# Performance work log

Hardware: AMD Instinct MI355X
Metric: run time of the kernel (lower is better)

The kernel has to match this reference:

```python
import jax, jax.numpy as jnp
import numpy as np

DIM = 2048
HQ = 32
HKV = 8
HEAD_DIM = DIM // HQ          # 64
GROUP = HQ // HKV             # 4 q-heads per kv-head
B, S = 2, 2048


def setup_inputs() -> dict:
    key = jax.random.key(0)
    ks = jax.random.split(key, 12)
    sc_in = 1.0 / np.sqrt(DIM)   # lecun_normal fan-in scaling
    inp = {
        "q": jax.random.normal(ks[0], (B, S, DIM), jnp.float32),
        "k": jax.random.normal(ks[1], (B, S, DIM), jnp.float32),
        "v": jax.random.normal(ks[2], (B, S, DIM), jnp.float32),
        # causal 0/1 mask: module computes scores -= 1/mask + 1, so 0 -> -inf (masked), 1 -> -2 (softmax-invariant shift)
        "mask": jnp.tril(jnp.ones((S, S), jnp.int32)),
        "Wq": jax.random.normal(ks[3], (DIM, HQ * HEAD_DIM), jnp.float32) * sc_in,
        "bq": jnp.zeros((HQ * HEAD_DIM,), jnp.float32),
        "Wk": jax.random.normal(ks[4], (DIM, HKV * HEAD_DIM), jnp.float32) * sc_in,
        "bk": jnp.zeros((HKV * HEAD_DIM,), jnp.float32),
        "Wv": jax.random.normal(ks[5], (DIM, HKV * HEAD_DIM), jnp.float32) * sc_in,
        "bv": jnp.zeros((HKV * HEAD_DIM,), jnp.float32),
        "Wo": jax.random.normal(ks[6], (DIM, DIM), jnp.float32) * (1.0 / np.sqrt(DIM)),
        "bo": jnp.zeros((DIM,), jnp.float32),
    }
    return inp


def reference(q, k, v, mask, Wq, bq, Wk, bk, Wv, bv, Wo, bo):
    b, s, _ = q.shape
    # projections -> per-head layout
    qx = (q @ Wq + bq).reshape(b, s, HKV, GROUP, HEAD_DIM)   # grouped q-heads
    kx = (k @ Wk + bk).reshape(b, s, HKV, HEAD_DIM)
    vx = (v @ Wv + bv).reshape(b, s, HKV, HEAD_DIM)
    # scores[b, h, g, i, j] = q_i . k_j ; same math as repeating kv heads GROUP times
    scores = jnp.einsum('bihgd,bjhd->bhgij', qx, kx) / jnp.sqrt(
        jnp.asarray(HEAD_DIM, qx.dtype))
    # module's masking: scores -= 1/mask + 1  (mask==0 -> -inf, mask==1 -> -2)
    scores = scores - (1.0 / mask.astype(scores.dtype) + 1.0)
    probs = jax.nn.softmax(scores, axis=-1)
    out = jnp.einsum('bhgij,bjhd->bihgd', probs, vx).reshape(b, s, DIM)
    out = out @ Wo + bo
    return out
```

## Files before the change

kernel.cpp:

```cpp
#include <hip/hip_runtime.h>

typedef unsigned short u16;
typedef unsigned int u32;
typedef __attribute__((ext_vector_type(8))) short short8v;
typedef __attribute__((ext_vector_type(4))) float f32x4;

#define DIM 2048
#define HQN 32
#define HKVN 8
#define HD 64
#define BB 2
#define SS 2048
#define MTOT (BB*SS)
#define NKV (HKVN*HD)
#define QSCL 0.18033688011112042f

__device__ __forceinline__ u16 f2bf(float f){
  u32 u = __float_as_uint(f);
  u += 0x7FFFu + ((u >> 16) & 1u);
  return (u16)(u >> 16);
}

__device__ __forceinline__ u32 cvtpk(float a, float b){
  u32 r; asm("v_cvt_pk_bf16_f32 %0, %1, %2" : "=v"(r) : "v"(a), "v"(b)); return r;
}

__device__ __forceinline__ void gload_lds16(const void* g, void* l){
  __builtin_amdgcn_global_load_lds((const __attribute__((address_space(1))) u32*)g,
                                   (__attribute__((address_space(3))) u32*)l, 16, 0, 0);
}

#define WAITVM_(N) asm volatile("s_waitcnt vmcnt(" #N ")" ::: "memory")
#define WAITVM(N) WAITVM_(N)
#define BARF()    do { asm volatile("" ::: "memory"); __builtin_amdgcn_s_barrier(); asm volatile("" ::: "memory"); } while(0)
#define MF(a,b,cc) __builtin_amdgcn_mfma_f32_16x16x32_bf16((a),(b),(cc),0,0,0)

__global__ __launch_bounds__(256) void cast3_kernel(const float4* __restrict__ q,
                                                    const float4* __restrict__ k,
                                                    const float4* __restrict__ v,
                                                    u16* __restrict__ qo,
                                                    u16* __restrict__ ko,
                                                    u16* __restrict__ vo, int n4){
  const int z = blockIdx.y;
  const float4* in = z==0 ? q : (z==1 ? k : v);
  u16* out = z==0 ? qo : (z==1 ? ko : vo);
  int i = blockIdx.x*256 + threadIdx.x;
  if (i < n4){
    float4 f = in[i];
    union { u16 s[4]; unsigned long long u; } r;
    r.s[0]=f2bf(f.x); r.s[1]=f2bf(f.y); r.s[2]=f2bf(f.z); r.s[3]=f2bf(f.w);
    *(unsigned long long*)(out + (size_t)i*4) = r.u;
  }
}

__global__ __launch_bounds__(256) void transpose4_kernel(const float* __restrict__ Wq,
                                                         const float* __restrict__ Wk,
                                                         const float* __restrict__ Wv,
                                                         const float* __restrict__ Wo,
                                                         u16* __restrict__ WqT,
                                                         u16* __restrict__ WkT,
                                                         u16* __restrict__ WvT,
                                                         u16* __restrict__ WoT){
  const int z = blockIdx.z;
  const float* W = z==0?Wq:(z==1?Wk:(z==2?Wv:Wo));
  u16* WT = z==0?WqT:(z==1?WkT:(z==2?WvT:WoT));
  const int N = (z==1||z==2) ? NKV : DIM;
  const int K = DIM;
  int n0 = blockIdx.x*32, k0 = blockIdx.y*32;
  if (n0 >= N) return;
  __shared__ float tile[32][33];
  int tx = threadIdx.x & 31, ty = threadIdx.x >> 5;
  #pragma unroll
  for (int i=0;i<4;i++){
    int kk = ty + i*8;
    tile[kk][tx] = W[(size_t)(k0+kk)*N + n0 + tx];
  }
  __syncthreads();
  #pragma unroll
  for (int i=0;i<4;i++){
    int n = ty + i*8;
    WT[(size_t)(n0+n)*K + k0 + tx] = f2bf(tile[tx][n]);
  }
}

__global__ __launch_bounds__(512, 1) void gemm_qkv_kernel(const u16* __restrict__ Aq,
                                                          const u16* __restrict__ Ak,
                                                          const u16* __restrict__ Av,
                                                          const u16* __restrict__ BT,
                                                          const float* __restrict__ bq,
                                                          const float* __restrict__ bk,
                                                          const float* __restrict__ bv,
                                                          u16* __restrict__ Qp,
                                                          u16* __restrict__ Kp,
                                                          u16* __restrict__ Vp){
  __shared__ __align__(16) u16 lds[65536];
  char* ldsb = (char*)lds;
  const int t = threadIdx.x, lane = t & 63, w = t >> 6;
  const int wm = w >> 2, wn = w & 3, g = lane >> 4, c = lane & 15;
  int bid = blockIdx.x;
  bid = (bid & 7)*24 + (bid >> 3);
  const int mt = bid / 12, nt = bid - mt*12;
  const int m0 = mt*256, n0 = nt*256;
  const int seg = (n0 >= 2560) ? 2 : (n0 >= 2048 ? 1 : 0);
  const u16* A = seg==0 ? Aq : (seg==1 ? Ak : Av);
  const float* bias = seg==0 ? bq : (seg==1 ? bk : bv);
  const int nbase = seg==0 ? 0 : (seg==1 ? 2048 : 2560);

  const int rA = t >> 3;
  const int kc = ((t & 7) ^ (rA & 7)) * 8;
  const u16* gA = A  + (size_t)(m0 + rA)*DIM + kc;
  const u16* gB = BT + (size_t)(n0 + ((rA>>5)<<6) + (rA & 31))*DIM + kc;

  const u32 ko0 = (u32)((g*16) ^ ((c&7)<<4));
  const u32 ko1 = (u32)((64 + g*16) ^ ((c&7)<<4));
  const u32 aoff = wm*8192 + c*128;
  const u32 boff = wn*4096 + c*128;

#define STGA_(PA, KT, ABASE) do{ \
    gload_lds16(gA + (size_t)(KT)*64 + (size_t)((PA)*64)*DIM,       ldsb + (ABASE) + (PA)*16384 + t*16); \
    gload_lds16(gA + (size_t)(KT)*64 + (size_t)((PA)*64+128)*DIM,   ldsb + (ABASE) + (PA)*16384 + 8192 + t*16); }while(0)
#define STGB_(PB, KT, BBASE) do{ \
    gload_lds16(gB + (size_t)(KT)*64 + (size_t)((PB)*32)*DIM,       ldsb + (BBASE) + (PB)*16384 + t*16); \
    gload_lds16(gB + (size_t)(KT)*64 + (size_t)((PB)*32+128)*DIM,   ldsb + (BBASE) + (PB)*16384 + 8192 + t*16); }while(0)
#define LD8(OFF) (*(const short8v*)(ldsb + (OFF)))

  const f32x4 fzero = {0.f,0.f,0.f,0.f};
  f32x4 acc[8][4];
  #pragma unroll
  for (int i=0;i<8;i++)
    #pragma unroll
    for (int j=0;j<4;j++) acc[i][j] = fzero;

#define RD_A(PABASE) do{ _Pragma("unroll") for (int q=0;q<4;q++){ \
    a_[q][0] = LD8((PABASE) + aoff + q*2048 + ko0); \
    a_[q][1] = LD8((PABASE) + aoff + q*2048 + ko1); } }while(0)
#define RD_B(DST, PBBASE) do{ _Pragma("unroll") for (int s=0;s<2;s++){ \
    DST[s][0] = LD8((PBBASE) + boff + s*2048 + ko0); \
    DST[s][1] = LD8((PBBASE) + boff + s*2048 + ko1); } }while(0)

#define MM16(BSRC, FM0, FN0) do{ __builtin_amdgcn_s_setprio(1); \
    _Pragma("unroll") for (int q=0;q<4;q++) \
      _Pragma("unroll") for (int s=0;s<2;s++){ \
        acc[(FM0)+q][(FN0)+s] = MF(a_[q][0], BSRC[s][0], acc[(FM0)+q][(FN0)+s]); \
        acc[(FM0)+q][(FN0)+s] = MF(a_[q][1], BSRC[s][1], acc[(FM0)+q][(FN0)+s]); } \
    __builtin_amdgcn_s_setprio(0); }while(0)

#define QSTEP(TT, CUR, DOSTG, TAIL) do{ \
    const u32 AC = (CUR)*32768,  BC2 = 65536 + (CUR)*32768; \
    const u32 AN = (CUR^1)*32768, BN2 = 65536 + (CUR^1)*32768; \
    short8v a_[4][2], b0_[2][2], b1_[2][2]; \
     \
    RD_A(AC); RD_B(b0_, BC2); \
    if (DOSTG) STGA_(0, (TT)+1, AN); \
    MM16(b0_, 0, 0); \
    if (TAIL) { WAITVM(2); } else { WAITVM(4); } \
    BARF(); \
     \
    RD_B(b1_, BC2 + 16384); \
    if (DOSTG) STGB_(0, (TT)+1, BN2); \
    MM16(b1_, 0, 2); \
    if (TAIL) { WAITVM(0); } else { WAITVM(4); } \
    BARF(); \
     \
    RD_A(AC + 16384); \
    if (DOSTG) STGB_(1, (TT)+1, BN2); \
    MM16(b1_, 4, 2); \
    BARF(); \
     \
    if (DOSTG) STGA_(1, (TT)+1, AN); \
    MM16(b0_, 4, 0); \
    if (!TAIL) { WAITVM(4); } \
    BARF(); \
  }while(0)

  STGA_(0, 0, 0); STGB_(0, 0, 65536); STGB_(1, 0, 65536); STGA_(1, 0, 0);
  WAITVM(4);
  BARF();

  #pragma unroll 1
  for (int tt = 0; tt < 30; tt += 2){
    QSTEP(tt,   0, 1, 0);
    QSTEP(tt+1, 1, 1, 0);
  }
  QSTEP(30, 0, 1, 0);
  QSTEP(31, 1, 0, 1);
#undef QSTEP

  WAITVM(0);
  __syncthreads();

  u16* st = lds + w*8192;
  const float osc = (seg == 0) ? QSCL : 1.0f;
  if (seg == 2){
    #pragma unroll
    for (int fm=0; fm<8; fm++){
      #pragma unroll
      for (int fn=0; fn<4; fn++){
        float bvv = bias[n0 - nbase + wn*64 + fn*16 + c];
        int vbase = (fm>>1)*2048 + fn*512 + (g*16 + c)*8 + (fm&1)*4;
        *(u32*)&st[vbase]     = cvtpk(acc[fm][fn][0]+bvv, acc[fm][fn][1]+bvv);
        *(u32*)&st[vbase + 2] = cvtpk(acc[fm][fn][2]+bvv, acc[fm][fn][3]+bvv);
      }
    }
  } else {
    #pragma unroll
    for (int fm=0; fm<8; fm++){
      #pragma unroll
      for (int fn=0; fn<4; fn++){
        float bvv = bias[n0 - nbase + wn*64 + fn*16 + c];
        int sbase = (fm>>1)*2048 + ((fm&1)*2 + (fn>>1))*512 + (c>>2)*128 + (fn&1)*4 + (c&3);
        #pragma unroll
        for (int r=0; r<4; r++)
          st[sbase + (4*g + r)*8] = f2bf((acc[fm][fn][r] + bvv)*osc);
      }
    }
  }
  __syncthreads();
  {
    const int bb = m0 >> 11;
    const int st0 = ((m0 & 2047) >> 5) + wm*4;
    u16* dst;
    if (seg == 0)      dst = Qp + (((size_t)bb*HQN  + (n0>>6)        + wn) << 17);
    else if (seg == 1) dst = Kp + (((size_t)bb*HKVN + ((n0-2048)>>6) + wn) << 17);
    else               dst = Vp + (((size_t)bb*HKVN + ((n0-2560)>>6) + wn) << 17);
    dst += (size_t)st0*2048;
    #pragma unroll
    for (int i=0;i<16;i++)
      *(short8v*)(dst + lane*8 + i*512) = *(const short8v*)(st + lane*8 + i*512);
  }
#undef STGA_
#undef STGB_
#undef RD_A
#undef RD_B
#undef MM16
#undef LD8
}

__global__ __launch_bounds__(512, 1) void gemm_o_kernel(const u16* __restrict__ A,
                                                        const u16* __restrict__ BT,
                                                        const float* __restrict__ bias,
                                                        float* __restrict__ C){
  __shared__ __align__(16) u16 lds[49152];
  char* ldsb = (char*)lds;
  const int t = threadIdx.x, lane = t & 63, w = t >> 6;
  const int wm = w >> 2, wn = w & 3, g = lane >> 4, c = lane & 15;
  int bid = blockIdx.x;
  bid = (bid & 7)*32 + (bid >> 3);
  const int m0 = (bid >> 4)*256, n0 = (bid & 15)*128;

  const int rA = t >> 3;
  const int kc = ((t & 7) ^ (rA & 7)) * 8;
  const u16* gA = A  + (size_t)(m0 + rA)*DIM + kc;
  const u16* gB = BT + (size_t)(n0 + rA)*DIM + kc;

  const u32 ko0 = (u32)((g*16) ^ ((c&7)<<4));
  const u32 ko1 = (u32)((64 + g*16) ^ ((c&7)<<4));
  const u32 aoff = wm*8192 + c*128;
  const u32 boffo = wn*4096 + c*128;

#define STGA_(PA, KT, ABASE) do{ \
    gload_lds16(gA + (size_t)(KT)*64 + (size_t)((PA)*64)*DIM,       ldsb + (ABASE) + (PA)*16384 + t*16); \
    gload_lds16(gA + (size_t)(KT)*64 + (size_t)((PA)*64+128)*DIM,   ldsb + (ABASE) + (PA)*16384 + 8192 + t*16); }while(0)
#define STGB_O(KT, BBASE) do{ \
    gload_lds16(gB + (size_t)(KT)*64,                     ldsb + (BBASE) + t*16); \
    gload_lds16(gB + (size_t)(KT)*64 + (size_t)64*DIM,    ldsb + (BBASE) + 8192 + t*16); }while(0)
#define LD8(OFF) (*(const short8v*)(ldsb + (OFF)))

  const f32x4 fzero = {0.f,0.f,0.f,0.f};
  f32x4 acc[8][2];
  #pragma unroll
  for (int i=0;i<8;i++){ acc[i][0] = fzero; acc[i][1] = fzero; }

#define RD_A(PABASE) do{ _Pragma("unroll") for (int q=0;q<4;q++){ \
    a_[q][0] = LD8((PABASE) + aoff + q*2048 + ko0); \
    a_[q][1] = LD8((PABASE) + aoff + q*2048 + ko1); } }while(0)
#define RD_BO(BBASE) do{ _Pragma("unroll") for (int s=0;s<2;s++){ \
    b_[s][0] = LD8((BBASE) + boffo + s*2048 + ko0); \
    b_[s][1] = LD8((BBASE) + boffo + s*2048 + ko1); } }while(0)

#define MMO(FM0) do{ __builtin_amdgcn_s_setprio(1); \
    _Pragma("unroll") for (int q=0;q<4;q++) \
      _Pragma("unroll") for (int s=0;s<2;s++){ \
        acc[(FM0)+q][s] = MF(a_[q][0], b_[s][0], acc[(FM0)+q][s]); \
        acc[(FM0)+q][s] = MF(a_[q][1], b_[s][1], acc[(FM0)+q][s]); } \
    __builtin_amdgcn_s_setprio(0); }while(0)

#define OSTEP(TT, CUR, DOSTG, TAIL) do{ \
    const u32 AC = (CUR)*32768,  BC2 = 65536 + (CUR)*16384; \
    const u32 AN = (CUR^1)*32768, BN2 = 65536 + (CUR^1)*16384; \
    short8v a_[4][2], b_[2][2]; \
     \
    RD_A(AC); RD_BO(BC2); \
    if (DOSTG) { STGA_(0, (TT)+1, AN); STGB_O((TT)+1, BN2); } \
    MMO(0); \
    if (TAIL) { WAITVM(0); } else { WAITVM(4); } \
    BARF(); \
     \
    RD_A(AC + 16384); \
    if (DOSTG) STGA_(1, (TT)+1, AN); \
    MMO(4); \
    if (!TAIL) { WAITVM(2); } \
    BARF(); \
  }while(0)

  STGA_(0, 0, 0); STGB_O(0, 65536); STGA_(1, 0, 0);
  WAITVM(2);
  BARF();

  #pragma unroll 1
  for (int tt = 0; tt < 30; tt += 2){
    OSTEP(tt,   0, 1, 0);
    OSTEP(tt+1, 1, 1, 0);
  }
  OSTEP(30, 0, 1, 0);
  OSTEP(31, 1, 0, 1);
#undef OSTEP

  #pragma unroll
  for (int fm=0; fm<8; fm++){
    #pragma unroll
    for (int s=0; s<2; s++){
      int n = n0 + wn*32 + s*16 + c;
      float bvv = bias[n];
      #pragma unroll
      for (int r=0; r<4; r++){
        int m = m0 + wm*128 + fm*16 + 4*g + r;
        C[(size_t)m*DIM + n] = acc[fm][s][r] + bvv;
      }
    }
  }
#undef STGA_
#undef STGB_O
#undef RD_A
#undef RD_BO
#undef MMO
#undef LD8
}

__global__ __launch_bounds__(256) void attn_kernel(const u16* __restrict__ Qp,
                                                   const u16* __restrict__ Kp,
                                                   const u16* __restrict__ Vp,
                                                   u16* __restrict__ Aout){
  const int bid = blockIdx.x;
  const int grp = bid & 15;
  const int T   = 63 - (bid >> 4);
  const int b   = grp >> 3;
  const int hkv = grp & 7;
  const int t = threadIdx.x;
  const int lane = t & 63, w = t >> 6;
  const int g = lane >> 4, c = lane & 15;
  const int hq = hkv*4 + w;

  __shared__ __align__(16) u16 ring[4][2][2048];

  const u16* Kb = Kp + (((size_t)b*HKVN + hkv) << 17);
  const u16* Vb = Vp + (((size_t)b*HKVN + hkv) << 17);
  const u16* Qb = Qp + (((size_t)b*HQN + hq) << 17);
  const f32x4 fzero = {0.f,0.f,0.f,0.f};

  short8v qf[2][2];
  {
    const u16* qs = Qb + (size_t)T*2048 + lane*8;
    qf[0][0] = *(const short8v*)(qs);
    qf[0][1] = *(const short8v*)(qs + 512);
    qf[1][0] = *(const short8v*)(qs + 1024);
    qf[1][1] = *(const short8v*)(qs + 1536);
  }
  float l_r[2] = {0.f, 0.f};
  f32x4 o[2][4];
  #pragma unroll
  for (int qi=0; qi<2; qi++)
    #pragma unroll
    for (int f=0; f<4; f++) o[qi][f] = fzero;

  #pragma unroll
  for (int s=0; s<3; s++){
    const int tc = s > T ? T : s;
    gload_lds16(Kb + (size_t)tc*2048 + t*8, &ring[s][0][t*8]);
    gload_lds16(Vb + (size_t)tc*2048 + t*8, &ring[s][1][t*8]);
  }

  for (int kt = 0; kt <= T; kt += 4){
    #pragma unroll
    for (int s4 = 0; s4 < 4; ++s4){
      const int kt_ = kt + s4;
      if (kt_ > T) break;
      WAITVM(4);
      BARF();
      short8v kf0 = *(const short8v*)&ring[s4][0][lane*8];
      short8v kf1 = *(const short8v*)&ring[s4][0][512 + lane*8];
      short8v kf2 = *(const short8v*)&ring[s4][0][1024 + lane*8];
      short8v kf3 = *(const short8v*)&ring[s4][0][1536 + lane*8];
      short8v vf0 = *(const short8v*)&ring[s4][1][lane*8];
      short8v vf1 = *(const short8v*)&ring[s4][1][512 + lane*8];
      short8v vf2 = *(const short8v*)&ring[s4][1][1024 + lane*8];
      short8v vf3 = *(const short8v*)&ring[s4][1][1536 + lane*8];
      {
        const int tc = (kt_+3) > T ? T : (kt_+3);
        const int sn = (s4+3) & 3;
        gload_lds16(Kb + (size_t)tc*2048 + t*8, &ring[sn][0][t*8]);
        gload_lds16(Vb + (size_t)tc*2048 + t*8, &ring[sn][1][t*8]);
      }
      const bool diag = (kt_ == T);
      #pragma unroll
      for (int qi=0; qi<2; qi++){
        f32x4 s0 = fzero, s1 = fzero;
        __builtin_amdgcn_s_setprio(1);
        s0 = MF(kf0, qf[qi][0], s0);
        s0 = MF(kf1, qf[qi][1], s0);
        s1 = MF(kf2, qf[qi][0], s1);
        s1 = MF(kf3, qf[qi][1], s1);
        __builtin_amdgcn_s_setprio(0);
        float p0[4], p1[4];
        #pragma unroll
        for (int r=0; r<4; r++){
          p0[r] = __builtin_amdgcn_exp2f(s0[r]);
          p1[r] = __builtin_amdgcn_exp2f(s1[r]);
        }
        if (diag){
          const int qloc = qi*16 + c;
          #pragma unroll
          for (int r=0; r<4; r++){
            if (4*g + r      > qloc) p0[r] = 0.f;
            if (16 + 4*g + r > qloc) p1[r] = 0.f;
          }
        }
        l_r[qi] += (p0[0]+p0[1]) + (p0[2]+p0[3]) + (p1[0]+p1[1]) + (p1[2]+p1[3]);
        union { u32 u[4]; short8v v; } pu;
        pu.u[0] = cvtpk(p0[0], p0[1]);
        pu.u[1] = cvtpk(p0[2], p0[3]);
        pu.u[2] = cvtpk(p1[0], p1[1]);
        pu.u[3] = cvtpk(p1[2], p1[3]);
        __builtin_amdgcn_s_setprio(1);
        o[qi][0] = MF(pu.v, vf0, o[qi][0]);
        o[qi][1] = MF(pu.v, vf1, o[qi][1]);
        o[qi][2] = MF(pu.v, vf2, o[qi][2]);
        o[qi][3] = MF(pu.v, vf3, o[qi][3]);
        __builtin_amdgcn_s_setprio(0);
      }
    }
  }

  #pragma unroll
  for (int qi=0; qi<2; qi++){
    float ls = l_r[qi];
    ls += __shfl_xor(ls, 16);
    ls += __shfl_xor(ls, 32);
    float li = 1.0f / ls;
    float lf[4];
    #pragma unroll
    for (int r=0; r<4; r++) lf[r] = __shfl(li, 4*g + r);
    #pragma unroll
    for (int f=0; f<4; f++){
      #pragma unroll
      for (int r=0; r<4; r++){
        int q = T*32 + qi*16 + 4*g + r;
        Aout[((size_t)b*SS + q)*DIM + hq*HD + f*16 + c] = f2bf(o[qi][f][r]*lf[r]);
      }
    }
  }
}

extern "C" void kernel_launch(void* const* d_in, const int* in_sizes, int n_in,
                              void* d_out, int out_size, void* d_ws, size_t ws_size,
                              hipStream_t stream){
  const float* q  = (const float*)d_in[0];
  const float* k  = (const float*)d_in[1];
  const float* v  = (const float*)d_in[2];
  const float* Wq = (const float*)d_in[4];
  const float* bq = (const float*)d_in[5];
  const float* Wk = (const float*)d_in[6];
  const float* bk = (const float*)d_in[7];
  const float* Wv = (const float*)d_in[8];
  const float* bv = (const float*)d_in[9];
  const float* Wo = (const float*)d_in[10];
  const float* bo = (const float*)d_in[11];
  float* out = (float*)d_out;

  char* ws = (char*)d_ws;
  u16* q_bf = (u16*)ws; ws += (size_t)MTOT*DIM*2;
  u16* k_bf = (u16*)ws; ws += (size_t)MTOT*DIM*2;
  u16* v_bf = (u16*)ws; ws += (size_t)MTOT*DIM*2;
  u16* WqT  = (u16*)ws; ws += (size_t)DIM*DIM*2;
  u16* WkT  = (u16*)ws; ws += (size_t)NKV*DIM*2;
  u16* WvT  = (u16*)ws; ws += (size_t)NKV*DIM*2;
  u16* WoT  = (u16*)ws; ws += (size_t)DIM*DIM*2;
  u16* Qp   = (u16*)ws; ws += (size_t)MTOT*DIM*2;
  u16* Kp   = (u16*)ws; ws += (size_t)MTOT*NKV*2;
  u16* Vp   = (u16*)ws; ws += (size_t)MTOT*NKV*2;
  u16* attn = (u16*)ws; ws += (size_t)MTOT*DIM*2;

  const int n4 = MTOT*DIM/4;
  cast3_kernel<<<dim3(n4/256, 3), 256, 0, stream>>>((const float4*)q, (const float4*)k,
                                                    (const float4*)v, q_bf, k_bf, v_bf, n4);
  transpose4_kernel<<<dim3(DIM/32, DIM/32, 4), 256, 0, stream>>>(Wq, Wk, Wv, Wo,
                                                                 WqT, WkT, WvT, WoT);
  gemm_qkv_kernel<<<192, 512, 0, stream>>>(q_bf, k_bf, v_bf, WqT,
                                           bq, bk, bv, Qp, Kp, Vp);
  attn_kernel<<<1024, 256, 0, stream>>>(Qp, Kp, Vp, attn);
  gemm_o_kernel<<<256, 512, 0, stream>>>(attn, WoT, bo, out);
}
```

Baseline: 188.4 us.

## Process two adjacent query tiles per attention block with 512 threads sharing K/V

Each attention block now has 8 waves covering two consecutive 32-row query tiles for the same kv-head, so every K/V tile staged in LDS serves twice as many waves. Global-to-LDS loading is split, with half the threads fetching K and half V. Block ordering is remapped so heavy and light tile pairs interleave. The grid is halved to 512 blocks, and waves of the lower tile sit idle for the final K/V step, which adds a little imbalance and lowers the number of independent blocks.

```diff
diff --git a/kernel.cpp b/kernel.cpp
--- a/kernel.cpp
+++ b/kernel.cpp
@@ -337,19 +337,23 @@
 #undef LD8
 }
 
-__global__ __launch_bounds__(256) void attn_kernel(const u16* __restrict__ Qp,
+__global__ __launch_bounds__(512) void attn_kernel(const u16* __restrict__ Qp,
                                                    const u16* __restrict__ Kp,
                                                    const u16* __restrict__ Vp,
                                                    u16* __restrict__ Aout){
   const int bid = blockIdx.x;
   const int grp = bid & 15;
-  const int T   = 63 - (bid >> 4);
+  const int j   = bid >> 4;
+  const int Tp  = (j < 16) ? j : 47 - j;
+  const int TB  = 2*Tp;
+  const int TMAX = TB + 1;
   const int b   = grp >> 3;
   const int hkv = grp & 7;
   const int t = threadIdx.x;
   const int lane = t & 63, w = t >> 6;
   const int g = lane >> 4, c = lane & 15;
-  const int hq = hkv*4 + w;
+  const int hq = hkv*4 + (w & 3);
+  const int Tw = TB + (w >> 2);
 
   __shared__ __align__(16) u16 ring[4][2][2048];
 
@@ -360,7 +364,7 @@
 
   short8v qf[2][2];
   {
-    const u16* qs = Qb + (size_t)T*2048 + lane*8;
+    const u16* qs = Qb + (size_t)Tw*2048 + lane*8;
     qf[0][0] = *(const short8v*)(qs);
     qf[0][1] = *(const short8v*)(qs + 512);
     qf[1][0] = *(const short8v*)(qs + 1024);
@@ -375,68 +379,70 @@
 
   #pragma unroll
   for (int s=0; s<3; s++){
-    const int tc = s > T ? T : s;
-    gload_lds16(Kb + (size_t)tc*2048 + t*8, &ring[s][0][t*8]);
-    gload_lds16(Vb + (size_t)tc*2048 + t*8, &ring[s][1][t*8]);
-  }
-
-  for (int kt = 0; kt <= T; kt += 4){
+    const int tc = s > TMAX ? TMAX : s;
+    if (t < 256) gload_lds16(Kb + (size_t)tc*2048 + t*8,        &ring[s][0][t*8]);
+    else         gload_lds16(Vb + (size_t)tc*2048 + (t-256)*8,  &ring[s][1][(t-256)*8]);
+  }
+
+  for (int kt = 0; kt <= TMAX; kt += 4){
     #pragma unroll
     for (int s4 = 0; s4 < 4; ++s4){
       const int kt_ = kt + s4;
-      if (kt_ > T) break;
-      WAITVM(4);
+      if (kt_ > TMAX) break;
+      WAITVM(2);
       BARF();
-      short8v kf0 = *(const short8v*)&ring[s4][0][lane*8];
-      short8v kf1 = *(const short8v*)&ring[s4][0][512 + lane*8];
-      short8v kf2 = *(const short8v*)&ring[s4][0][1024 + lane*8];
-      short8v kf3 = *(const short8v*)&ring[s4][0][1536 + lane*8];
-      short8v vf0 = *(const short8v*)&ring[s4][1][lane*8];
-      short8v vf1 = *(const short8v*)&ring[s4][1][512 + lane*8];
-      short8v vf2 = *(const short8v*)&ring[s4][1][1024 + lane*8];
-      short8v vf3 = *(const short8v*)&ring[s4][1][1536 + lane*8];
       {
-        const int tc = (kt_+3) > T ? T : (kt_+3);
+        const int tc = (kt_+3) > TMAX ? TMAX : (kt_+3);
         const int sn = (s4+3) & 3;
-        gload_lds16(Kb + (size_t)tc*2048 + t*8, &ring[sn][0][t*8]);
-        gload_lds16(Vb + (size_t)tc*2048 + t*8, &ring[sn][1][t*8]);
+        if (t < 256) gload_lds16(Kb + (size_t)tc*2048 + t*8,       &ring[sn][0][t*8]);
+        else         gload_lds16(Vb + (size_t)tc*2048 + (t-256)*8, &ring[sn][1][(t-256)*8]);
       }
-      const bool diag = (kt_ == T);
-      #pragma unroll
-      for (int qi=0; qi<2; qi++){
-        f32x4 s0 = fzero, s1 = fzero;
-        __builtin_amdgcn_s_setprio(1);
-        s0 = MF(kf0, qf[qi][0], s0);
-        s0 = MF(kf1, qf[qi][1], s0);
-        s1 = MF(kf2, qf[qi][0], s1);
-        s1 = MF(kf3, qf[qi][1], s1);
-        __builtin_amdgcn_s_setprio(0);
-        float p0[4], p1[4];
+      if (kt_ <= Tw){
+        short8v kf0 = *(const short8v*)&ring[s4][0][lane*8];
+        short8v kf1 = *(const short8v*)&ring[s4][0][512 + lane*8];
+        short8v kf2 = *(const short8v*)&ring[s4][0][1024 + lane*8];
+        short8v kf3 = *(const short8v*)&ring[s4][0][1536 + lane*8];
+        short8v vf0 = *(const short8v*)&ring[s4][1][lane*8];
+        short8v vf1 = *(const short8v*)&ring[s4][1][512 + lane*8];
+        short8v vf2 = *(const short8v*)&ring[s4][1][1024 + lane*8];
+        short8v vf3 = *(const short8v*)&ring[s4][1][1536 + lane*8];
+        const bool diag = (kt_ == Tw);
         #pragma unroll
-        for (int r=0; r<4; r++){
-          p0[r] = __builtin_amdgcn_exp2f(s0[r]);
-          p1[r] = __builtin_amdgcn_exp2f(s1[r]);
-        }
-        if (diag){
-          const int qloc = qi*16 + c;
+        for (int qi=0; qi<2; qi++){
+          f32x4 s0 = fzero, s1 = fzero;
+          __builtin_amdgcn_s_setprio(1);
+          s0 = MF(kf0, qf[qi][0], s0);
+          s0 = MF(kf1, qf[qi][1], s0);
+          s1 = MF(kf2, qf[qi][0], s1);
+          s1 = MF(kf3, qf[qi][1], s1);
+          __builtin_amdgcn_s_setprio(0);
+          float p0[4], p1[4];
           #pragma unroll
           for (int r=0; r<4; r++){
-            if (4*g + r      > qloc) p0[r] = 0.f;
-            if (16 + 4*g + r > qloc) p1[r] = 0.f;
+            p0[r] = __builtin_amdgcn_exp2f(s0[r]);
+            p1[r] = __builtin_amdgcn_exp2f(s1[r]);
           }
+          if (diag){
+            const int qloc = qi*16 + c;
+            #pragma unroll
+            for (int r=0; r<4; r++){
+              if (4*g + r      > qloc) p0[r] = 0.f;
+              if (16 + 4*g + r > qloc) p1[r] = 0.f;
+            }
+          }
+          l_r[qi] += (p0[0]+p0[1]) + (p0[2]+p0[3]) + (p1[0]+p1[1]) + (p1[2]+p1[3]);
+          union { u32 u[4]; short8v v; } pu;
+          pu.u[0] = cvtpk(p0[0], p0[1]);
+          pu.u[1] = cvtpk(p0[2], p0[3]);
+          pu.u[2] = cvtpk(p1[0], p1[1]);
+          pu.u[3] = cvtpk(p1[2], p1[3]);
+          __builtin_amdgcn_s_setprio(1);
+          o[qi][0] = MF(pu.v, vf0, o[qi][0]);
+          o[qi][1] = MF(pu.v, vf1, o[qi][1]);
+          o[qi][2] = MF(pu.v, vf2, o[qi][2]);
+          o[qi][3] = MF(pu.v, vf3, o[qi][3]);
+          __builtin_amdgcn_s_setprio(0);
         }
-        l_r[qi] += (p0[0]+p0[1]) + (p0[2]+p0[3]) + (p1[0]+p1[1]) + (p1[2]+p1[3]);
-        union { u32 u[4]; short8v v; } pu;
-        pu.u[0] = cvtpk(p0[0], p0[1]);
-        pu.u[1] = cvtpk(p0[2], p0[3]);
-        pu.u[2] = cvtpk(p1[0], p1[1]);
-        pu.u[3] = cvtpk(p1[2], p1[3]);
-        __builtin_amdgcn_s_setprio(1);
-        o[qi][0] = MF(pu.v, vf0, o[qi][0]);
-        o[qi][1] = MF(pu.v, vf1, o[qi][1]);
-        o[qi][2] = MF(pu.v, vf2, o[qi][2]);
-        o[qi][3] = MF(pu.v, vf3, o[qi][3]);
-        __builtin_amdgcn_s_setprio(0);
       }
     }
   }
@@ -454,7 +460,7 @@
     for (int f=0; f<4; f++){
       #pragma unroll
       for (int r=0; r<4; r++){
-        int q = T*32 + qi*16 + 4*g + r;
+        int q = Tw*32 + qi*16 + 4*g + r;
         Aout[((size_t)b*SS + q)*DIM + hq*HD + f*16 + c] = f2bf(o[qi][f][r]*lf[r]);
       }
     }
@@ -497,6 +503,6 @@
                                                                  WqT, WkT, WvT, WoT);
   gemm_qkv_kernel<<<192, 512, 0, stream>>>(q_bf, k_bf, v_bf, WqT,
                                            bq, bk, bv, Qp, Kp, Vp);
-  attn_kernel<<<1024, 256, 0, stream>>>(Qp, Kp, Vp, attn);
+  attn_kernel<<<512, 512, 0, stream>>>(Qp, Kp, Vp, attn);
   gemm_o_kernel<<<256, 512, 0, stream>>>(attn, WoT, bo, out);
 }
```

Measured after the change: 190.8 us. About the same (+1.2%).
